# Kernel tuning notes

Hardware: AMD Instinct MI355X
Metric: run time of the kernel (lower is better)

The kernel has to match this reference:

```python
import jax, jax.numpy as jnp
import numpy as np

EPS = 1e-12  # F.normalize default eps

def setup_inputs() -> dict:
    key = jax.random.key(0)
    k1, k2, k3, k4, k5, k6 = jax.random.split(key, 6)
    B, N, F_in, F_out = 8, 2048, 128, 128
    h = jax.random.normal(k1, (B, N, F_in), dtype=jnp.float32)
    # binary adjacency with avg degree ~32 (p = 32/2048)
    adj = (jax.random.uniform(k2, (B, N, N)) < (32.0 / N)).astype(jnp.float32)
    lim = 1.0 / np.sqrt(F_in)
    W_self = jax.random.uniform(k3, (F_in, F_out), minval=-lim, maxval=lim, dtype=jnp.float32)
    b_self = jax.random.uniform(k4, (F_out,), minval=-lim, maxval=lim, dtype=jnp.float32)
    W_neigh = jax.random.uniform(k5, (F_in, F_out), minval=-lim, maxval=lim, dtype=jnp.float32)
    b_neigh = jax.random.uniform(k6, (F_out,), minval=-lim, maxval=lim, dtype=jnp.float32)
    return {"h": h, "adj": adj, "W_self": W_self, "b_self": b_self,
            "W_neigh": W_neigh, "b_neigh": b_neigh}

def reference(h, adj, W_self, b_self, W_neigh, b_neigh):
    # Original builds (B,N,N,F) = adj[:, i, :, None] * h then mean over dim=-2.
    # mean divides by N (not degree), so aggregated = (adj @ h) / N. Fused form:
    N = h.shape[1]
    aggregated = jnp.einsum('bij,bjf->bif', adj, h) / N  # (B,N,F_in)
    out = h @ W_self + b_self + aggregated @ W_neigh + b_neigh
    out = jax.nn.relu(out)
    # F.normalize(p=2, dim=-1): x / max(||x||, eps)
    norm = jnp.linalg.norm(out, axis=-1, keepdims=True)
    out = out / jnp.maximum(norm, EPS)
    return out  # dropout(p=0.0) is identity
```

## Files before the change

### kernel.cpp

```cpp
#include <hip/hip_runtime.h>

typedef unsigned int u32;
typedef unsigned long long u64;

#define BATCH 8
#define NNODE 2048
#define FEAT  128
#define CAP   320

__global__ __launch_bounds__(256) void agg_sparse_kernel(
    const float* __restrict__ adj,
    const float* __restrict__ h,
    float* __restrict__ agg)
{
  __shared__ int sIdx[4][CAP];
  const int tid = threadIdx.x;
  const int l = tid & 63;
  const int w = tid >> 6;
  const int row = blockIdx.x * 4 + w;
  const int b = row >> 11;
  const float* arow = adj + (size_t)row * NNODE;
  const float* hB = h + (size_t)b * NNODE * FEAT;
  const int l2 = 2 * l;
  int* idx = sIdx[w];

  float4 vc[8];
#pragma unroll
  for (int i = 0; i < 8; i++)
    vc[i] = *(const float4*)(arow + i * 256 + l * 4);

  u32 mask = 0;
#pragma unroll
  for (int i = 0; i < 8; i++) {
    mask |= (vc[i].x != 0.0f ? 1u : 0u) << (i * 4 + 0);
    mask |= (vc[i].y != 0.0f ? 1u : 0u) << (i * 4 + 1);
    mask |= (vc[i].z != 0.0f ? 1u : 0u) << (i * 4 + 2);
    mask |= (vc[i].w != 0.0f ? 1u : 0u) << (i * 4 + 3);
  }
  const int cnt = __popc(mask);
  int s = cnt;
#pragma unroll
  for (int d = 1; d < 64; d <<= 1) {
    int t = __shfl_up(s, d);
    if (l >= d) s += t;
  }
  const int total = __shfl(s, 63);
  int pos = s - cnt;
  u32 m = mask;
  while (m) {
    int bb = __builtin_ctz(m);
    m &= m - 1;
    if (pos < CAP) idx[pos] = ((bb >> 2) << 8) + 4 * l + (bb & 3);
    pos++;
  }
  const int n = (total < CAP) ? total : CAP;

  float ax = 0.0f, ay = 0.0f;
  int i = 0;
  for (; i + 8 <= n; i += 8) {
    int4 j0 = *(const int4*)&idx[i];
    int4 j1 = *(const int4*)&idx[i + 4];
    float2 g0 = *(const float2*)(hB + (size_t)j0.x * FEAT + l2);
    float2 g1 = *(const float2*)(hB + (size_t)j0.y * FEAT + l2);
    float2 g2 = *(const float2*)(hB + (size_t)j0.z * FEAT + l2);
    float2 g3 = *(const float2*)(hB + (size_t)j0.w * FEAT + l2);
    float2 g4 = *(const float2*)(hB + (size_t)j1.x * FEAT + l2);
    float2 g5 = *(const float2*)(hB + (size_t)j1.y * FEAT + l2);
    float2 g6 = *(const float2*)(hB + (size_t)j1.z * FEAT + l2);
    float2 g7 = *(const float2*)(hB + (size_t)j1.w * FEAT + l2);
    ax += ((g0.x + g1.x) + (g2.x + g3.x)) + ((g4.x + g5.x) + (g6.x + g7.x));
    ay += ((g0.y + g1.y) + (g2.y + g3.y)) + ((g4.y + g5.y) + (g6.y + g7.y));
  }
  for (; i < n; i++) {
    int j = idx[i];
    const float2 g = *(const float2*)(hB + (size_t)j * FEAT + l2);
    ax += g.x; ay += g.y;
  }

  const float invN = 1.0f / (float)NNODE;
  float2 res;
  res.x = ax * invN;
  res.y = ay * invN;
  *(float2*)(agg + (size_t)row * FEAT + l2) = res;
}

#define APITCH 68
#define BPITCH 132

__global__ __launch_bounds__(256) void linear_kernel(
    const float* __restrict__ h,
    const float* __restrict__ agg,
    const float* __restrict__ Ws,
    const float* __restrict__ bs,
    const float* __restrict__ Wn,
    const float* __restrict__ bn,
    float* __restrict__ out)
{
  __shared__ float sA[64 * APITCH];
  __shared__ float sB[64 * BPITCH];

  const int tid = threadIdx.x;
  const int tx = tid & 15;
  const int rg = tid >> 4;
  const int r0 = blockIdx.x * 64;

  float acc[4][8];
#pragma unroll
  for (int r = 0; r < 4; r++)
#pragma unroll
    for (int c = 0; c < 8; c++) acc[r][c] = 0.0f;

  const int arl = tid >> 2;
  const int aq  = tid & 3;
  const int bkl = tid >> 2;
  const int bq  = tid & 3;

  for (int t = 0; t < 4; t++) {
    const float* Asrc = ((t < 2) ? h : agg) + (size_t)(t & 1) * 64;
    const float* Bsrc = (t < 2) ? (Ws + (size_t)(t * 64) * FEAT)
                                : (Wn + (size_t)((t - 2) * 64) * FEAT);
    __syncthreads();
    {
      const float* src = Asrc + (size_t)(r0 + arl) * FEAT + aq * 4;
#pragma unroll
      for (int ii = 0; ii < 4; ii++) {
        float4 vv = *(const float4*)(src + ii * 16);
        int kk = aq * 4 + ii * 16;
        sA[(kk + 0) * APITCH + arl] = vv.x;
        sA[(kk + 1) * APITCH + arl] = vv.y;
        sA[(kk + 2) * APITCH + arl] = vv.z;
        sA[(kk + 3) * APITCH + arl] = vv.w;
      }
    }
    {
      const float* src = Bsrc + (size_t)bkl * FEAT;
#pragma unroll
      for (int j = 0; j < 8; j++) {
        int cw = (bq + 4 * j) * 4;
        *(float4*)&sB[bkl * BPITCH + cw] = *(const float4*)(src + cw);
      }
    }
    __syncthreads();
#pragma unroll 4
    for (int k = 0; k < 64; k++) {
      float4 av = *(const float4*)&sA[k * APITCH + rg * 4];
      float4 b0 = *(const float4*)&sB[k * BPITCH + tx * 8];
      float4 b1 = *(const float4*)&sB[k * BPITCH + tx * 8 + 4];
      const float a[4] = {av.x, av.y, av.z, av.w};
      const float bb[8] = {b0.x, b0.y, b0.z, b0.w, b1.x, b1.y, b1.z, b1.w};
#pragma unroll
      for (int r = 0; r < 4; r++)
#pragma unroll
        for (int c = 0; c < 8; c++)
          acc[r][c] += a[r] * bb[c];
    }
  }

  float4 bsv0 = *(const float4*)(bs + tx * 8);
  float4 bsv1 = *(const float4*)(bs + tx * 8 + 4);
  float4 bnv0 = *(const float4*)(bn + tx * 8);
  float4 bnv1 = *(const float4*)(bn + tx * 8 + 4);
  float bias[8];
  bias[0] = bsv0.x + bnv0.x; bias[1] = bsv0.y + bnv0.y;
  bias[2] = bsv0.z + bnv0.z; bias[3] = bsv0.w + bnv0.w;
  bias[4] = bsv1.x + bnv1.x; bias[5] = bsv1.y + bnv1.y;
  bias[6] = bsv1.z + bnv1.z; bias[7] = bsv1.w + bnv1.w;

  float ss[4] = {0.f, 0.f, 0.f, 0.f};
#pragma unroll
  for (int r = 0; r < 4; r++)
#pragma unroll
    for (int c = 0; c < 8; c++) {
      float vv = acc[r][c] + bias[c];
      if (vv < 0.0f) vv = 0.0f;
      acc[r][c] = vv;
      ss[r] += vv * vv;
    }
#pragma unroll
  for (int r = 0; r < 4; r++) {
    float s = ss[r];
    s += __shfl_xor(s, 1);
    s += __shfl_xor(s, 2);
    s += __shfl_xor(s, 4);
    s += __shfl_xor(s, 8);
    float nrm = sqrtf(s);
    if (nrm < 1e-12f) nrm = 1e-12f;
    ss[r] = 1.0f / nrm;
  }
#pragma unroll
  for (int r = 0; r < 4; r++) {
    float* orow = out + (size_t)(r0 + rg * 4 + r) * FEAT + tx * 8;
    float4 w0, w1;
    w0.x = acc[r][0] * ss[r]; w0.y = acc[r][1] * ss[r];
    w0.z = acc[r][2] * ss[r]; w0.w = acc[r][3] * ss[r];
    w1.x = acc[r][4] * ss[r]; w1.y = acc[r][5] * ss[r];
    w1.z = acc[r][6] * ss[r]; w1.w = acc[r][7] * ss[r];
    *(float4*)(orow) = w0;
    *(float4*)(orow + 4) = w1;
  }
}

extern "C" void kernel_launch(void* const* d_in, const int* in_sizes, int n_in,
                              void* d_out, int out_size, void* d_ws, size_t ws_size,
                              hipStream_t stream) {
  const float* h   = (const float*)d_in[0];
  const float* adj = (const float*)d_in[1];
  const float* Ws  = (const float*)d_in[2];
  const float* bs  = (const float*)d_in[3];
  const float* Wn  = (const float*)d_in[4];
  const float* bn  = (const float*)d_in[5];
  float* out = (float*)d_out;
  float* agg = (float*)d_ws;

  (void)in_sizes; (void)n_in; (void)out_size; (void)ws_size;

  agg_sparse_kernel<<<dim3(BATCH * NNODE / 4), dim3(256), 0, stream>>>(adj, h, agg);
  linear_kernel<<<dim3(BATCH * NNODE / 64), dim3(256), 0, stream>>>(
      h, agg, Ws, bs, Wn, bn, out);
}
```

Before: 234.0 us.

## Reorder GNN layer to transform first, then aggregate with fused epilogue

Uses associativity, (adj@h)@Wn = adj@(h@Wn), so the dense GEMM now runs first and produces P = h@Ws + biases and G = h@Wn, split across a 2-wide grid. The sparse aggregation kernel then gathers rows of G and applies the add, ReLU and L2 normalization in the same pass, removing the separate agg buffer round trip. Adjacency loads and output stores become nontemporal. The cost is an extra intermediate buffer (P and G) written and read back, and a changed floating-point summation order.

```diff
diff --git a/kernel.cpp b/kernel.cpp
--- a/kernel.cpp
+++ b/kernel.cpp
@@ -2,99 +2,26 @@
 
 typedef unsigned int u32;
 typedef unsigned long long u64;
+typedef float f4v __attribute__((ext_vector_type(4)));
+typedef float f2v __attribute__((ext_vector_type(2)));
 
 #define BATCH 8
 #define NNODE 2048
 #define FEAT  128
 #define CAP   320
 
-__global__ __launch_bounds__(256) void agg_sparse_kernel(
-    const float* __restrict__ adj,
-    const float* __restrict__ h,
-    float* __restrict__ agg)
-{
-  __shared__ int sIdx[4][CAP];
-  const int tid = threadIdx.x;
-  const int l = tid & 63;
-  const int w = tid >> 6;
-  const int row = blockIdx.x * 4 + w;
-  const int b = row >> 11;
-  const float* arow = adj + (size_t)row * NNODE;
-  const float* hB = h + (size_t)b * NNODE * FEAT;
-  const int l2 = 2 * l;
-  int* idx = sIdx[w];
-
-  float4 vc[8];
-#pragma unroll
-  for (int i = 0; i < 8; i++)
-    vc[i] = *(const float4*)(arow + i * 256 + l * 4);
-
-  u32 mask = 0;
-#pragma unroll
-  for (int i = 0; i < 8; i++) {
-    mask |= (vc[i].x != 0.0f ? 1u : 0u) << (i * 4 + 0);
-    mask |= (vc[i].y != 0.0f ? 1u : 0u) << (i * 4 + 1);
-    mask |= (vc[i].z != 0.0f ? 1u : 0u) << (i * 4 + 2);
-    mask |= (vc[i].w != 0.0f ? 1u : 0u) << (i * 4 + 3);
-  }
-  const int cnt = __popc(mask);
-  int s = cnt;
-#pragma unroll
-  for (int d = 1; d < 64; d <<= 1) {
-    int t = __shfl_up(s, d);
-    if (l >= d) s += t;
-  }
-  const int total = __shfl(s, 63);
-  int pos = s - cnt;
-  u32 m = mask;
-  while (m) {
-    int bb = __builtin_ctz(m);
-    m &= m - 1;
-    if (pos < CAP) idx[pos] = ((bb >> 2) << 8) + 4 * l + (bb & 3);
-    pos++;
-  }
-  const int n = (total < CAP) ? total : CAP;
-
-  float ax = 0.0f, ay = 0.0f;
-  int i = 0;
-  for (; i + 8 <= n; i += 8) {
-    int4 j0 = *(const int4*)&idx[i];
-    int4 j1 = *(const int4*)&idx[i + 4];
-    float2 g0 = *(const float2*)(hB + (size_t)j0.x * FEAT + l2);
-    float2 g1 = *(const float2*)(hB + (size_t)j0.y * FEAT + l2);
-    float2 g2 = *(const float2*)(hB + (size_t)j0.z * FEAT + l2);
-    float2 g3 = *(const float2*)(hB + (size_t)j0.w * FEAT + l2);
-    float2 g4 = *(const float2*)(hB + (size_t)j1.x * FEAT + l2);
-    float2 g5 = *(const float2*)(hB + (size_t)j1.y * FEAT + l2);
-    float2 g6 = *(const float2*)(hB + (size_t)j1.z * FEAT + l2);
-    float2 g7 = *(const float2*)(hB + (size_t)j1.w * FEAT + l2);
-    ax += ((g0.x + g1.x) + (g2.x + g3.x)) + ((g4.x + g5.x) + (g6.x + g7.x));
-    ay += ((g0.y + g1.y) + (g2.y + g3.y)) + ((g4.y + g5.y) + (g6.y + g7.y));
-  }
-  for (; i < n; i++) {
-    int j = idx[i];
-    const float2 g = *(const float2*)(hB + (size_t)j * FEAT + l2);
-    ax += g.x; ay += g.y;
-  }
-
-  const float invN = 1.0f / (float)NNODE;
-  float2 res;
-  res.x = ax * invN;
-  res.y = ay * invN;
-  *(float2*)(agg + (size_t)row * FEAT + l2) = res;
-}
 
 #define APITCH 68
 #define BPITCH 132
 
-__global__ __launch_bounds__(256) void linear_kernel(
+__global__ __launch_bounds__(256) void gemm_pg_kernel(
     const float* __restrict__ h,
-    const float* __restrict__ agg,
     const float* __restrict__ Ws,
     const float* __restrict__ bs,
     const float* __restrict__ Wn,
     const float* __restrict__ bn,
-    float* __restrict__ out)
+    float* __restrict__ P,
+    float* __restrict__ G)
 {
   __shared__ float sA[64 * APITCH];
   __shared__ float sB[64 * BPITCH];
@@ -103,6 +30,9 @@
   const int tx = tid & 15;
   const int rg = tid >> 4;
   const int r0 = blockIdx.x * 64;
+  const int half = blockIdx.y;
+  const float* __restrict__ W = half ? Wn : Ws;
+  float* __restrict__ op = half ? G : P;
 
   float acc[4][8];
 #pragma unroll
@@ -115,13 +45,10 @@
   const int bkl = tid >> 2;
   const int bq  = tid & 3;
 
-  for (int t = 0; t < 4; t++) {
-    const float* Asrc = ((t < 2) ? h : agg) + (size_t)(t & 1) * 64;
-    const float* Bsrc = (t < 2) ? (Ws + (size_t)(t * 64) * FEAT)
-                                : (Wn + (size_t)((t - 2) * 64) * FEAT);
+  for (int t = 0; t < 2; t++) {
     __syncthreads();
     {
-      const float* src = Asrc + (size_t)(r0 + arl) * FEAT + aq * 4;
+      const float* src = h + (size_t)(r0 + arl) * FEAT + t * 64 + aq * 4;
 #pragma unroll
       for (int ii = 0; ii < 4; ii++) {
         float4 vv = *(const float4*)(src + ii * 16);
@@ -133,7 +60,7 @@
       }
     }
     {
-      const float* src = Bsrc + (size_t)bkl * FEAT;
+      const float* src = W + (size_t)(t * 64 + bkl) * FEAT;
 #pragma unroll
       for (int j = 0; j < 8; j++) {
         int cw = (bq + 4 * j) * 4;
@@ -156,48 +83,126 @@
     }
   }
 
-  float4 bsv0 = *(const float4*)(bs + tx * 8);
-  float4 bsv1 = *(const float4*)(bs + tx * 8 + 4);
-  float4 bnv0 = *(const float4*)(bn + tx * 8);
-  float4 bnv1 = *(const float4*)(bn + tx * 8 + 4);
   float bias[8];
-  bias[0] = bsv0.x + bnv0.x; bias[1] = bsv0.y + bnv0.y;
-  bias[2] = bsv0.z + bnv0.z; bias[3] = bsv0.w + bnv0.w;
-  bias[4] = bsv1.x + bnv1.x; bias[5] = bsv1.y + bnv1.y;
-  bias[6] = bsv1.z + bnv1.z; bias[7] = bsv1.w + bnv1.w;
-
-  float ss[4] = {0.f, 0.f, 0.f, 0.f};
-#pragma unroll
-  for (int r = 0; r < 4; r++)
-#pragma unroll
-    for (int c = 0; c < 8; c++) {
-      float vv = acc[r][c] + bias[c];
-      if (vv < 0.0f) vv = 0.0f;
-      acc[r][c] = vv;
-      ss[r] += vv * vv;
-    }
+  if (half == 0) {
+    float4 b0 = *(const float4*)(bs + tx * 8);
+    float4 b1 = *(const float4*)(bs + tx * 8 + 4);
+    float4 c0 = *(const float4*)(bn + tx * 8);
+    float4 c1 = *(const float4*)(bn + tx * 8 + 4);
+    bias[0] = b0.x + c0.x; bias[1] = b0.y + c0.y;
+    bias[2] = b0.z + c0.z; bias[3] = b0.w + c0.w;
+    bias[4] = b1.x + c1.x; bias[5] = b1.y + c1.y;
+    bias[6] = b1.z + c1.z; bias[7] = b1.w + c1.w;
+  } else {
+#pragma unroll
+    for (int c = 0; c < 8; c++) bias[c] = 0.0f;
+  }
 #pragma unroll
   for (int r = 0; r < 4; r++) {
-    float s = ss[r];
-    s += __shfl_xor(s, 1);
-    s += __shfl_xor(s, 2);
-    s += __shfl_xor(s, 4);
-    s += __shfl_xor(s, 8);
-    float nrm = sqrtf(s);
-    if (nrm < 1e-12f) nrm = 1e-12f;
-    ss[r] = 1.0f / nrm;
-  }
-#pragma unroll
-  for (int r = 0; r < 4; r++) {
-    float* orow = out + (size_t)(r0 + rg * 4 + r) * FEAT + tx * 8;
+    float* orow = op + (size_t)(r0 + rg * 4 + r) * FEAT + tx * 8;
     float4 w0, w1;
-    w0.x = acc[r][0] * ss[r]; w0.y = acc[r][1] * ss[r];
-    w0.z = acc[r][2] * ss[r]; w0.w = acc[r][3] * ss[r];
-    w1.x = acc[r][4] * ss[r]; w1.y = acc[r][5] * ss[r];
-    w1.z = acc[r][6] * ss[r]; w1.w = acc[r][7] * ss[r];
+    w0.x = acc[r][0] + bias[0]; w0.y = acc[r][1] + bias[1];
+    w0.z = acc[r][2] + bias[2]; w0.w = acc[r][3] + bias[3];
+    w1.x = acc[r][4] + bias[4]; w1.y = acc[r][5] + bias[5];
+    w1.z = acc[r][6] + bias[6]; w1.w = acc[r][7] + bias[7];
     *(float4*)(orow) = w0;
     *(float4*)(orow + 4) = w1;
   }
+}
+
+__global__ __launch_bounds__(256) void fused_agg_kernel(
+    const float* __restrict__ adj,
+    const float* __restrict__ G,
+    const float* __restrict__ P,
+    float* __restrict__ out)
+{
+  __shared__ int sIdx[4][CAP];
+  const int tid = threadIdx.x;
+  const int l = tid & 63;
+  const int w = tid >> 6;
+  const int row = blockIdx.x * 4 + w;
+  const int b = row >> 11;
+  const float* arow = adj + (size_t)row * NNODE;
+  const float* gB = G + (size_t)b * NNODE * FEAT;
+  const int l2 = 2 * l;
+  int* idx = sIdx[w];
+
+  const float2 pv = *(const float2*)(P + (size_t)row * FEAT + l2);
+
+  f4v vc[8];
+#pragma unroll
+  for (int i = 0; i < 8; i++)
+    vc[i] = __builtin_nontemporal_load((const f4v*)(arow + i * 256 + l * 4));
+
+  u32 mask = 0;
+#pragma unroll
+  for (int i = 0; i < 8; i++) {
+    mask |= (vc[i].x != 0.0f ? 1u : 0u) << (i * 4 + 0);
+    mask |= (vc[i].y != 0.0f ? 1u : 0u) << (i * 4 + 1);
+    mask |= (vc[i].z != 0.0f ? 1u : 0u) << (i * 4 + 2);
+    mask |= (vc[i].w != 0.0f ? 1u : 0u) << (i * 4 + 3);
+  }
+  const int cnt = __popc(mask);
+  int s = cnt;
+#pragma unroll
+  for (int d = 1; d < 64; d <<= 1) {
+    int t = __shfl_up(s, d);
+    if (l >= d) s += t;
+  }
+  const int total = __shfl(s, 63);
+  int pos = s - cnt;
+  u32 m = mask;
+  while (m) {
+    int bb = __builtin_ctz(m);
+    m &= m - 1;
+    if (pos < CAP) idx[pos] = ((bb >> 2) << 8) + 4 * l + (bb & 3);
+    pos++;
+  }
+  const int n = (total < CAP) ? total : CAP;
+
+  float ax = 0.0f, ay = 0.0f;
+  int i = 0;
+  for (; i + 8 <= n; i += 8) {
+    int4 j0 = *(const int4*)&idx[i];
+    int4 j1 = *(const int4*)&idx[i + 4];
+    float2 g0 = *(const float2*)(gB + (size_t)j0.x * FEAT + l2);
+    float2 g1 = *(const float2*)(gB + (size_t)j0.y * FEAT + l2);
+    float2 g2 = *(const float2*)(gB + (size_t)j0.z * FEAT + l2);
+    float2 g3 = *(const float2*)(gB + (size_t)j0.w * FEAT + l2);
+    float2 g4 = *(const float2*)(gB + (size_t)j1.x * FEAT + l2);
+    float2 g5 = *(const float2*)(gB + (size_t)j1.y * FEAT + l2);
+    float2 g6 = *(const float2*)(gB + (size_t)j1.z * FEAT + l2);
+    float2 g7 = *(const float2*)(gB + (size_t)j1.w * FEAT + l2);
+    ax += ((g0.x + g1.x) + (g2.x + g3.x)) + ((g4.x + g5.x) + (g6.x + g7.x));
+    ay += ((g0.y + g1.y) + (g2.y + g3.y)) + ((g4.y + g5.y) + (g6.y + g7.y));
+  }
+  for (; i < n; i++) {
+    int j = idx[i];
+    const float2 g = *(const float2*)(gB + (size_t)j * FEAT + l2);
+    ax += g.x; ay += g.y;
+  }
+
+  const float invN = 1.0f / (float)NNODE;
+  float px = pv.x + ax * invN;
+  float py = pv.y + ay * invN;
+  px = px > 0.0f ? px : 0.0f;
+  py = py > 0.0f ? py : 0.0f;
+
+  float ssum = px * px + py * py;
+  ssum += __shfl_xor(ssum, 1);
+  ssum += __shfl_xor(ssum, 2);
+  ssum += __shfl_xor(ssum, 4);
+  ssum += __shfl_xor(ssum, 8);
+  ssum += __shfl_xor(ssum, 16);
+  ssum += __shfl_xor(ssum, 32);
+  float nrm = sqrtf(ssum);
+  if (nrm < 1e-12f) nrm = 1e-12f;
+  const float inv = 1.0f / nrm;
+
+  f2v res;
+  res.x = px * inv;
+  res.y = py * inv;
+  __builtin_nontemporal_store(res, (f2v*)(out + (size_t)row * FEAT + l2));
 }
 
 extern "C" void kernel_launch(void* const* d_in, const int* in_sizes, int n_in,
@@ -210,11 +215,13 @@
   const float* Wn  = (const float*)d_in[4];
   const float* bn  = (const float*)d_in[5];
   float* out = (float*)d_out;
-  float* agg = (float*)d_ws;
+  float* P = (float*)d_ws;
+  float* G = P + (size_t)BATCH * NNODE * FEAT;
 
   (void)in_sizes; (void)n_in; (void)out_size; (void)ws_size;
 
-  agg_sparse_kernel<<<dim3(BATCH * NNODE / 4), dim3(256), 0, stream>>>(adj, h, agg);
-  linear_kernel<<<dim3(BATCH * NNODE / 64), dim3(256), 0, stream>>>(
-      h, agg, Ws, bs, Wn, bn, out);
+  gemm_pg_kernel<<<dim3(BATCH * NNODE / 64, 2), dim3(256), 0, stream>>>(
+      h, Ws, bs, Wn, bn, P, G);
+  fused_agg_kernel<<<dim3(BATCH * NNODE / 4), dim3(256), 0, stream>>>(
+      adj, G, P, out);
 }
```

After: 228.3 us. -2.4%, faster.
